# Kernel optimization log

Measured on AMD Instinct MI355X. Metric: run time of the kernel, lower is better.

Reference implementation:

```python
import jax, jax.numpy as jnp
import numpy as np

# Representation: lvals=[0,1] -> nreps NL=2, dim DIM=1+3=4; mult=8; kqv conv out_mult=3*mult
N, K, EDGE_DIM, HID = 10000, 16, 32, 64
MULT, NL, DIM = 8, 2, 4
OUT_MULT = 3 * MULT
E = N * K
NHEADS = 4
HEAD_DIM = MULT * DIM // NHEADS  # 8


def setup_inputs() -> dict:
    key = jax.random.key(0)
    ks = jax.random.split(key, 9)
    out_flat = NL * NL * MULT * OUT_MULT  # 768
    return {
        "basis1": jax.random.normal(ks[0], (E, DIM, NL), jnp.float32),
        "basis2": jax.random.normal(ks[1], (E, NL, DIM), jnp.float32),
        "edge_feats": jax.random.normal(ks[2], (E, EDGE_DIM), jnp.float32),
        "f": jax.random.normal(ks[3], (N, MULT, DIM), jnp.float32),
        "W1": jax.random.normal(ks[4], (HID, EDGE_DIM), jnp.float32) / np.sqrt(EDGE_DIM).astype(np.float32),
        "b1": jnp.zeros((HID,), jnp.float32),
        "W2": jax.random.normal(ks[5], (out_flat, HID), jnp.float32) / np.sqrt(HID).astype(np.float32),
        "b2": jnp.zeros((out_flat,), jnp.float32),
        "neighbor_idx": jax.random.randint(ks[6], (N, K), 0, N, dtype=jnp.int32),
    }


def reference(basis1, basis2, edge_feats, f, W1, b1, W2, b2, neighbor_idx):
    src = neighbor_idx.reshape(-1)  # (E,) source node per edge
    # RadialWeight: 2-layer MLP edge_feats -> per-edge TP weights (E, NL*OUT_MULT, NL*MULT)
    h = jax.nn.relu(edge_feats @ W1.T + b1)
    rw = (h @ W2.T + b2).reshape(E, NL * OUT_MULT, NL * MULT)
    # EquivariantConvolution: gather + small batched matmuls
    f_src = f[src]  # (E, MULT, DIM)
    tmp = jnp.einsum('emd,edl->eml', f_src, basis1).reshape(E, NL * MULT, 1)
    tmp = (rw @ tmp).reshape(E, OUT_MULT, NL)
    kqv = jnp.einsum('eml,eld->emd', tmp, basis2)  # (E, 3*MULT, DIM)
    # split fused k/q/v along multiplicity (repr_h.rep2.mult = 3*mult)
    k_, q_, v_ = jnp.split(kqv.reshape(N, K, OUT_MULT, DIM), 3, axis=2)  # each (N,K,MULT,DIM)
    k_ = k_.reshape(N, K, NHEADS, HEAD_DIM)
    v_ = v_.reshape(N, K, NHEADS, HEAD_DIM)
    q_node = q_.reshape(N, K, NHEADS, HEAD_DIM).mean(axis=1)  # per-node query (N,H,hd)
    scale = HEAD_DIM ** -0.5
    scores = jnp.einsum('nhd,nkhd->nhk', q_node, k_) * scale  # (N,H,K)
    w = jax.nn.softmax(scores, axis=-1)
    out = jnp.einsum('nhk,nkhd->nhd', w, v_)  # (N,H,hd)
    return out.reshape(N, MULT, DIM)
```

## Files before the change

kernel.cpp:

```cpp
#include <hip/hip_runtime.h>
#include <hip/hip_bf16.h>
#include <math.h>

#define N_NODES 10000
#define KNBR    16
#define EDGEF   32
#define HID     64
#define MULT    8
#define NL      2
#define DIM     4
#define OUT_MULT 24
#define NHEADS  4
#define HEAD_DIM 8
#define E_TOT   (N_NODES*KNBR)

#define EPB 128
#define TPB 256
#define NODES_PB 8
#define NSLICE 33

typedef float    f32x4 __attribute__((ext_vector_type(4)));
typedef _Float16 f16x8 __attribute__((ext_vector_type(8)));

#define BF1_HALVES (4*64*8)
#define BF2_HALVES (3*NSLICE*64*8)
#define WS_HALVES  (BF1_HALVES + BF2_HALVES)

__global__ __launch_bounds__(256)
void esa_prep(const float* __restrict__ W1, const float* __restrict__ W2,
              const float* __restrict__ b2, _Float16* __restrict__ wsh)
{
    int i = blockIdx.x * 256 + threadIdx.x;
    if (i >= WS_HALVES) return;
    float v;
    if (i < BF1_HALVES) {
        int j = i & 7, lane = (i >> 3) & 63, t = i >> 9;
        int k = ((lane >> 4) << 3) + j;
        int n = (t << 4) + (lane & 15);
        v = W1[n * EDGEF + k];
    } else {
        int i2 = i - BF1_HALVES;
        int j = i2 & 7, lane = (i2 >> 3) & 63;
        int st = i2 >> 9;
        int s = st % NSLICE, t = st / NSLICE;
        int k = (s << 5) + ((lane >> 4) << 3) + j;
        int n = (t << 4) + (lane & 15);
        if (k < 1024)      v = W2[(n * 16 + (k >> 6)) * HID + (k & 63)];
        else if (k < 1040) v = b2[n * 16 + (k - 1024)];
        else               v = 0.f;
    }
    wsh[i] = (_Float16)v;
}

__global__ __launch_bounds__(TPB)
void esa_main(const float* __restrict__ basis1, const float* __restrict__ basis2,
              const float* __restrict__ edge_feats, const float* __restrict__ f,
              const float* __restrict__ b1, const int* __restrict__ nbr,
              const _Float16* __restrict__ wsh, float* __restrict__ out)
{
    __shared__ __align__(16) unsigned char smem[53248];
    float*    t2  = (float*)smem;
    _Float16* hls = (_Float16*)(smem + 26624);
    _Float16* tpl = (_Float16*)(smem + 45056);
    float*    b2l = (float*)(smem + 49152);

    const int tid  = threadIdx.x;
    const int eb   = blockIdx.x * EPB;
    const int lane = tid & 63;
    const int w    = tid >> 6;
    const int lo   = lane & 15, hi = lane >> 4;

    {
        int el = tid >> 1, hf = tid & 1;
        int e  = eb + el;
        int src = nbr[e];
        const float4* b1p = (const float4*)(basis1 + (size_t)e * 8);
        float4 u0 = b1p[0], u1 = b1p[1];
        float bl0[4] = {u0.x, u0.z, u1.x, u1.z};
        float bl1[4] = {u0.y, u0.w, u1.y, u1.w};
        const float4* fp = (const float4*)(f + (size_t)src * 32 + hf * 16);
        _Float16 tpv[8];
        #pragma unroll
        for (int mm = 0; mm < 4; ++mm) {
            float4 fv = fp[mm];
            float a0 = fv.x*bl0[0] + fv.y*bl0[1] + fv.z*bl0[2] + fv.w*bl0[3];
            float a1 = fv.x*bl1[0] + fv.y*bl1[1] + fv.z*bl1[2] + fv.w*bl1[3];
            tpv[mm*2+0] = (_Float16)a0;
            tpv[mm*2+1] = (_Float16)a1;
        }
        *(f16x8*)(tpl + el*16 + hf*8) = *(f16x8*)tpv;
        float4 b2v = ((const float4*)(basis2 + (size_t)e * 8))[hf];
        *((float4*)(b2l + el*8) + hf) = b2v;
    }

    {
        float b1v[4];
        #pragma unroll
        for (int t = 0; t < 4; ++t) b1v[t] = b1[t*16 + lo];
        f16x8 afr[2];
        #pragma unroll
        for (int mt = 0; mt < 2; ++mt) {
            size_t eg = (size_t)(eb + w*32 + mt*16 + lo);
            const float4* p = (const float4*)(edge_feats + eg*32 + hi*8);
            float4 x0 = p[0], x1 = p[1];
            f16x8 a;
            a[0]=(_Float16)x0.x; a[1]=(_Float16)x0.y; a[2]=(_Float16)x0.z; a[3]=(_Float16)x0.w;
            a[4]=(_Float16)x1.x; a[5]=(_Float16)x1.y; a[6]=(_Float16)x1.z; a[7]=(_Float16)x1.w;
            afr[mt] = a;
        }
        #pragma unroll
        for (int t = 0; t < 4; ++t) {
            f16x8 bfr = *(const f16x8*)(wsh + ((size_t)(t*64 + lane)) * 8);
            #pragma unroll
            for (int mt = 0; mt < 2; ++mt) {
                f32x4 acc = {0.f, 0.f, 0.f, 0.f};
                acc = __builtin_amdgcn_mfma_f32_16x16x32_f16(afr[mt], bfr, acc, 0, 0, 0);
                #pragma unroll
                for (int r = 0; r < 4; ++r) {
                    float hv = acc[r] + b1v[t];
                    hv = hv > 0.f ? hv : 0.f;
                    int el = w*32 + mt*16 + hi*4 + r;
                    hls[el*72 + t*16 + lo] = (_Float16)hv;
                }
            }
        }
    }
    __syncthreads();

    {
        f32x4 acc[2][3];
        #pragma unroll
        for (int mt = 0; mt < 2; ++mt)
            #pragma unroll
            for (int t = 0; t < 3; ++t)
                acc[mt][t] = (f32x4){0.f, 0.f, 0.f, 0.f};

        const _Float16* Bf2 = wsh + BF1_HALVES;
        const int e0 = w*32 + lo;
        const int e1 = e0 + 16;
        const _Float16* hp0 = hls + e0*72 + hi*8;
        const _Float16* hp1 = hls + e1*72 + hi*8;
        f16x8 tp0a = *(const f16x8*)(tpl + e0*16);
        f16x8 tp0b = *(const f16x8*)(tpl + e0*16 + 8);
        f16x8 tp1a = *(const f16x8*)(tpl + e1*16);
        f16x8 tp1b = *(const f16x8*)(tpl + e1*16 + 8);

        #pragma unroll
        for (int sp = 0; sp < 16; ++sp) {
            _Float16 t0 = (sp < 8) ? tp0a[sp & 7] : tp0b[sp & 7];
            _Float16 t1 = (sp < 8) ? tp1a[sp & 7] : tp1b[sp & 7];
            f16x8 ts0 = {t0,t0,t0,t0,t0,t0,t0,t0};
            f16x8 ts1 = {t1,t1,t1,t1,t1,t1,t1,t1};
            #pragma unroll
            for (int sh = 0; sh < 2; ++sh) {
                const int s = sp*2 + sh;
                f16x8 bfr[3];
                #pragma unroll
                for (int t = 0; t < 3; ++t)
                    bfr[t] = *(const f16x8*)(Bf2 + ((size_t)((t*NSLICE + s)*64 + lane)) * 8);
                f16x8 h0 = *(const f16x8*)(hp0 + sh*32);
                f16x8 h1 = *(const f16x8*)(hp1 + sh*32);
                f16x8 a0 = h0 * ts0;
                f16x8 a1 = h1 * ts1;
                #pragma unroll
                for (int t = 0; t < 3; ++t) {
                    acc[0][t] = __builtin_amdgcn_mfma_f32_16x16x32_f16(a0, bfr[t], acc[0][t], 0, 0, 0);
                    acc[1][t] = __builtin_amdgcn_mfma_f32_16x16x32_f16(a1, bfr[t], acc[1][t], 0, 0, 0);
                }
            }
        }
        {
            f16x8 z = {(_Float16)0,(_Float16)0,(_Float16)0,(_Float16)0,
                       (_Float16)0,(_Float16)0,(_Float16)0,(_Float16)0};
            f16x8 a0 = (hi == 0) ? tp0a : (hi == 1) ? tp0b : z;
            f16x8 a1 = (hi == 0) ? tp1a : (hi == 1) ? tp1b : z;
            #pragma unroll
            for (int t = 0; t < 3; ++t) {
                f16x8 bfr = *(const f16x8*)(Bf2 + ((size_t)((t*NSLICE + 32)*64 + lane)) * 8);
                acc[0][t] = __builtin_amdgcn_mfma_f32_16x16x32_f16(a0, bfr, acc[0][t], 0, 0, 0);
                acc[1][t] = __builtin_amdgcn_mfma_f32_16x16x32_f16(a1, bfr, acc[1][t], 0, 0, 0);
            }
        }
        #pragma unroll
        for (int mt = 0; mt < 2; ++mt)
            #pragma unroll
            for (int t = 0; t < 3; ++t)
                #pragma unroll
                for (int r = 0; r < 4; ++r)
                    t2[(w*32 + mt*16 + hi*4 + r)*52 + t*16 + lo] = acc[mt][t][r];
    }
    __syncthreads();

    const int kk = lane >> 2, hh = lane & 3;
    #pragma unroll
    for (int it = 0; it < 2; ++it) {
        int nl = it*4 + w;
        int node = blockIdx.x * NODES_PB + nl;
        int el = nl*16 + kk;
        const float* trow = t2 + el*52;
        float4 tk = *(const float4*)(trow + hh*4);
        float4 tq = *(const float4*)(trow + 16 + hh*4);
        float4 tv = *(const float4*)(trow + 32 + hh*4);
        float4 bl0 = *(const float4*)(b2l + el*8);
        float4 bl1 = *(const float4*)(b2l + el*8 + 4);
        float k8[8], q8[8], v8[8];
        const float* B0 = (const float*)&bl0;
        const float* B1 = (const float*)&bl1;
        #pragma unroll
        for (int d = 0; d < 4; ++d) {
            k8[d]   = tk.x*B0[d] + tk.y*B1[d];
            k8[4+d] = tk.z*B0[d] + tk.w*B1[d];
            q8[d]   = tq.x*B0[d] + tq.y*B1[d];
            q8[4+d] = tq.z*B0[d] + tq.w*B1[d];
            v8[d]   = tv.x*B0[d] + tv.y*B1[d];
            v8[4+d] = tv.z*B0[d] + tv.w*B1[d];
        }
        float qn[8];
        #pragma unroll
        for (int i = 0; i < 8; ++i) qn[i] = q8[i];
        #pragma unroll
        for (int m = 4; m <= 32; m <<= 1)
            #pragma unroll
            for (int i = 0; i < 8; ++i) qn[i] += __shfl_xor(qn[i], m);
        float s = 0.f;
        #pragma unroll
        for (int i = 0; i < 8; ++i) s += qn[i]*k8[i];
        s *= 0.0220970869120796f;

        float mx = s;
        #pragma unroll
        for (int m = 4; m <= 32; m <<= 1) mx = fmaxf(mx, __shfl_xor(mx, m));
        float ex = __expf(s - mx);
        float den = ex;
        #pragma unroll
        for (int m = 4; m <= 32; m <<= 1) den += __shfl_xor(den, m);
        float wgt = ex / den;

        float o[8];
        #pragma unroll
        for (int i = 0; i < 8; ++i) o[i] = wgt * v8[i];
        #pragma unroll
        for (int m = 4; m <= 32; m <<= 1)
            #pragma unroll
            for (int i = 0; i < 8; ++i) o[i] += __shfl_xor(o[i], m);
        if (kk == 0) {
            float4* dst = (float4*)(out + (size_t)node*32 + hh*8);
            dst[0] = make_float4(o[0], o[1], o[2], o[3]);
            dst[1] = make_float4(o[4], o[5], o[6], o[7]);
        }
    }
}

extern "C" void kernel_launch(void* const* d_in, const int* in_sizes, int n_in,
                              void* d_out, int out_size, void* d_ws, size_t ws_size,
                              hipStream_t stream) {
    const float* basis1     = (const float*)d_in[0];
    const float* basis2     = (const float*)d_in[1];
    const float* edge_feats = (const float*)d_in[2];
    const float* f          = (const float*)d_in[3];
    const float* W1         = (const float*)d_in[4];
    const float* b1         = (const float*)d_in[5];
    const float* W2         = (const float*)d_in[6];
    const float* b2         = (const float*)d_in[7];
    const int*   nbr        = (const int*)d_in[8];
    float* out = (float*)d_out;
    _Float16* wsh = (_Float16*)d_ws;

    esa_prep<<<(WS_HALVES + 255)/256, 256, 0, stream>>>(W1, W2, b2, wsh);
    esa_main<<<E_TOT/EPB, TPB, 0, stream>>>(basis1, basis2, edge_feats, f,
                                            b1, nbr, wsh, out);
}
```

Before: 117.7 us.

## Split fused kernel into GEMM kernel and attention kernel via global scratch

Splits the fused kernel into two. The GEMM kernel writes per-edge intermediate t2 (E×48 floats) to global workspace, and a separate attention kernel reads it back along with basis2. This cuts shared memory from 52 KB to 22 KB and sets launch bounds for 4 blocks per CU, aiming for higher occupancy. In exchange it adds about 19 MB of global write and read traffic plus an extra kernel launch.

```diff
diff --git a/kernel.cpp b/kernel.cpp
--- a/kernel.cpp
+++ b/kernel.cpp
@@ -16,7 +16,6 @@
 
 #define EPB 128
 #define TPB 256
-#define NODES_PB 8
 #define NSLICE 33
 
 typedef float    f32x4 __attribute__((ext_vector_type(4)));
@@ -25,6 +24,7 @@
 #define BF1_HALVES (4*64*8)
 #define BF2_HALVES (3*NSLICE*64*8)
 #define WS_HALVES  (BF1_HALVES + BF2_HALVES)
+#define T2_OFF     131072
 
 __global__ __launch_bounds__(256)
 void esa_prep(const float* __restrict__ W1, const float* __restrict__ W2,
@@ -52,17 +52,15 @@
     wsh[i] = (_Float16)v;
 }
 
-__global__ __launch_bounds__(TPB)
-void esa_main(const float* __restrict__ basis1, const float* __restrict__ basis2,
-              const float* __restrict__ edge_feats, const float* __restrict__ f,
-              const float* __restrict__ b1, const int* __restrict__ nbr,
-              const _Float16* __restrict__ wsh, float* __restrict__ out)
+__global__ __launch_bounds__(TPB, 4)
+void esa_gemm(const float* __restrict__ basis1, const float* __restrict__ edge_feats,
+              const float* __restrict__ f, const float* __restrict__ b1,
+              const int* __restrict__ nbr, const _Float16* __restrict__ wsh,
+              float* __restrict__ t2g)
 {
-    __shared__ __align__(16) unsigned char smem[53248];
-    float*    t2  = (float*)smem;
-    _Float16* hls = (_Float16*)(smem + 26624);
-    _Float16* tpl = (_Float16*)(smem + 45056);
-    float*    b2l = (float*)(smem + 49152);
+    __shared__ __align__(16) unsigned char smem[22528];
+    _Float16* hls = (_Float16*)smem;
+    _Float16* tpl = (_Float16*)(smem + 18432);
 
     const int tid  = threadIdx.x;
     const int eb   = blockIdx.x * EPB;
@@ -89,8 +87,6 @@
             tpv[mm*2+1] = (_Float16)a1;
         }
         *(f16x8*)(tpl + el*16 + hf*8) = *(f16x8*)tpv;
-        float4 b2v = ((const float4*)(basis2 + (size_t)e * 8))[hf];
-        *((float4*)(b2l + el*8) + hf) = b2v;
     }
 
     {
@@ -187,67 +183,72 @@
             for (int t = 0; t < 3; ++t)
                 #pragma unroll
                 for (int r = 0; r < 4; ++r)
-                    t2[(w*32 + mt*16 + hi*4 + r)*52 + t*16 + lo] = acc[mt][t][r];
-    }
-    __syncthreads();
-
-    const int kk = lane >> 2, hh = lane & 3;
-    #pragma unroll
-    for (int it = 0; it < 2; ++it) {
-        int nl = it*4 + w;
-        int node = blockIdx.x * NODES_PB + nl;
-        int el = nl*16 + kk;
-        const float* trow = t2 + el*52;
-        float4 tk = *(const float4*)(trow + hh*4);
-        float4 tq = *(const float4*)(trow + 16 + hh*4);
-        float4 tv = *(const float4*)(trow + 32 + hh*4);
-        float4 bl0 = *(const float4*)(b2l + el*8);
-        float4 bl1 = *(const float4*)(b2l + el*8 + 4);
-        float k8[8], q8[8], v8[8];
-        const float* B0 = (const float*)&bl0;
-        const float* B1 = (const float*)&bl1;
-        #pragma unroll
-        for (int d = 0; d < 4; ++d) {
-            k8[d]   = tk.x*B0[d] + tk.y*B1[d];
-            k8[4+d] = tk.z*B0[d] + tk.w*B1[d];
-            q8[d]   = tq.x*B0[d] + tq.y*B1[d];
-            q8[4+d] = tq.z*B0[d] + tq.w*B1[d];
-            v8[d]   = tv.x*B0[d] + tv.y*B1[d];
-            v8[4+d] = tv.z*B0[d] + tv.w*B1[d];
-        }
-        float qn[8];
-        #pragma unroll
-        for (int i = 0; i < 8; ++i) qn[i] = q8[i];
-        #pragma unroll
-        for (int m = 4; m <= 32; m <<= 1)
-            #pragma unroll
-            for (int i = 0; i < 8; ++i) qn[i] += __shfl_xor(qn[i], m);
-        float s = 0.f;
-        #pragma unroll
-        for (int i = 0; i < 8; ++i) s += qn[i]*k8[i];
-        s *= 0.0220970869120796f;
-
-        float mx = s;
-        #pragma unroll
-        for (int m = 4; m <= 32; m <<= 1) mx = fmaxf(mx, __shfl_xor(mx, m));
-        float ex = __expf(s - mx);
-        float den = ex;
-        #pragma unroll
-        for (int m = 4; m <= 32; m <<= 1) den += __shfl_xor(den, m);
-        float wgt = ex / den;
-
-        float o[8];
-        #pragma unroll
-        for (int i = 0; i < 8; ++i) o[i] = wgt * v8[i];
-        #pragma unroll
-        for (int m = 4; m <= 32; m <<= 1)
-            #pragma unroll
-            for (int i = 0; i < 8; ++i) o[i] += __shfl_xor(o[i], m);
-        if (kk == 0) {
-            float4* dst = (float4*)(out + (size_t)node*32 + hh*8);
-            dst[0] = make_float4(o[0], o[1], o[2], o[3]);
-            dst[1] = make_float4(o[4], o[5], o[6], o[7]);
-        }
+                    t2g[(size_t)(eb + w*32 + mt*16 + hi*4 + r)*48 + t*16 + lo] = acc[mt][t][r];
+    }
+}
+
+__global__ __launch_bounds__(256)
+void esa_attn(const float* __restrict__ t2g, const float* __restrict__ basis2,
+              float* __restrict__ out)
+{
+    const int tid  = threadIdx.x;
+    const int w    = tid >> 6;
+    const int lane = tid & 63;
+    const int node = blockIdx.x * 4 + w;
+    const int kk   = lane >> 2, hh = lane & 3;
+    const int e    = node * KNBR + kk;
+
+    const float* trow = t2g + (size_t)e * 48;
+    float4 tk = *(const float4*)(trow + hh*4);
+    float4 tq = *(const float4*)(trow + 16 + hh*4);
+    float4 tv = *(const float4*)(trow + 32 + hh*4);
+    float4 bl0 = *(const float4*)(basis2 + (size_t)e * 8);
+    float4 bl1 = *(const float4*)(basis2 + (size_t)e * 8 + 4);
+
+    float k8[8], q8[8], v8[8];
+    const float* B0 = (const float*)&bl0;
+    const float* B1 = (const float*)&bl1;
+    #pragma unroll
+    for (int d = 0; d < 4; ++d) {
+        k8[d]   = tk.x*B0[d] + tk.y*B1[d];
+        k8[4+d] = tk.z*B0[d] + tk.w*B1[d];
+        q8[d]   = tq.x*B0[d] + tq.y*B1[d];
+        q8[4+d] = tq.z*B0[d] + tq.w*B1[d];
+        v8[d]   = tv.x*B0[d] + tv.y*B1[d];
+        v8[4+d] = tv.z*B0[d] + tv.w*B1[d];
+    }
+    float qn[8];
+    #pragma unroll
+    for (int i = 0; i < 8; ++i) qn[i] = q8[i];
+    #pragma unroll
+    for (int m = 4; m <= 32; m <<= 1)
+        #pragma unroll
+        for (int i = 0; i < 8; ++i) qn[i] += __shfl_xor(qn[i], m);
+    float s = 0.f;
+    #pragma unroll
+    for (int i = 0; i < 8; ++i) s += qn[i]*k8[i];
+    s *= 0.0220970869120796f;
+
+    float mx = s;
+    #pragma unroll
+    for (int m = 4; m <= 32; m <<= 1) mx = fmaxf(mx, __shfl_xor(mx, m));
+    float ex = __expf(s - mx);
+    float den = ex;
+    #pragma unroll
+    for (int m = 4; m <= 32; m <<= 1) den += __shfl_xor(den, m);
+    float wgt = ex / den;
+
+    float o[8];
+    #pragma unroll
+    for (int i = 0; i < 8; ++i) o[i] = wgt * v8[i];
+    #pragma unroll
+    for (int m = 4; m <= 32; m <<= 1)
+        #pragma unroll
+        for (int i = 0; i < 8; ++i) o[i] += __shfl_xor(o[i], m);
+    if (kk == 0) {
+        float4* dst = (float4*)(out + (size_t)node*32 + hh*8);
+        dst[0] = make_float4(o[0], o[1], o[2], o[3]);
+        dst[1] = make_float4(o[4], o[5], o[6], o[7]);
     }
 }
 
@@ -265,8 +266,9 @@
     const int*   nbr        = (const int*)d_in[8];
     float* out = (float*)d_out;
     _Float16* wsh = (_Float16*)d_ws;
+    float* t2g = (float*)((char*)d_ws + T2_OFF);
 
     esa_prep<<<(WS_HALVES + 255)/256, 256, 0, stream>>>(W1, W2, b2, wsh);
-    esa_main<<<E_TOT/EPB, TPB, 0, stream>>>(basis1, basis2, edge_feats, f,
-                                            b1, nbr, wsh, out);
-}
+    esa_gemm<<<E_TOT/EPB, TPB, 0, stream>>>(basis1, edge_feats, f, b1, nbr, wsh, t2g);
+    esa_attn<<<N_NODES/4, 256, 0, stream>>>(t2g, basis2, out);
+}
```

Result: slower. 126.3 us (+7.4%).

## Stage second-layer weight fragments through double-buffered LDS via async global-to-LDS loads

Applied to the files above, without the earlier changes.

Instead of every wave fetching the same second-layer weight fragments from global memory inside the MFMA loop, the four waves now cooperatively copy chunks of slices into two LDS buffers with global_load_lds. The next chunk is prefetched while the current one is consumed, with a block barrier per chunk. The aim is to remove redundant per-wave global/L1 traffic and hide load latency behind the MFMAs. It also loads the hidden activations into registers once, remaps the shared-memory layout (the output tile now overlaps the dead hidden buffer), pads the basis2 stride, and requests 3 blocks per CU in launch bounds. The cost is extra barriers and reliance on correct wait semantics for the async LDS loads.

```diff
diff --git a/kernel.cpp b/kernel.cpp
--- a/kernel.cpp
+++ b/kernel.cpp
@@ -6,18 +6,14 @@
 #define KNBR    16
 #define EDGEF   32
 #define HID     64
-#define MULT    8
-#define NL      2
-#define DIM     4
-#define OUT_MULT 24
-#define NHEADS  4
-#define HEAD_DIM 8
 #define E_TOT   (N_NODES*KNBR)
 
 #define EPB 128
 #define TPB 256
 #define NODES_PB 8
 #define NSLICE 33
+#define CHUNK 4
+#define NCHUNK 8
 
 typedef float    f32x4 __attribute__((ext_vector_type(4)));
 typedef _Float16 f16x8 __attribute__((ext_vector_type(8)));
@@ -52,23 +48,39 @@
     wsh[i] = (_Float16)v;
 }
 
-__global__ __launch_bounds__(TPB)
+__device__ __forceinline__ void issue16(const _Float16* g, unsigned char* l) {
+    __builtin_amdgcn_global_load_lds(
+        (const __attribute__((address_space(1))) void*)g,
+        (__attribute__((address_space(3))) void*)(void*)l, 16, 0, 0);
+}
+
+__global__ __launch_bounds__(TPB, 3)
 void esa_main(const float* __restrict__ basis1, const float* __restrict__ basis2,
               const float* __restrict__ edge_feats, const float* __restrict__ f,
               const float* __restrict__ b1, const int* __restrict__ nbr,
               const _Float16* __restrict__ wsh, float* __restrict__ out)
 {
     __shared__ __align__(16) unsigned char smem[53248];
+    _Float16* hls = (_Float16*)(smem + 24576);
+    _Float16* tpl = (_Float16*)(smem + 43008);
+    float*    b2l = (float*)(smem + 47104);
     float*    t2  = (float*)smem;
-    _Float16* hls = (_Float16*)(smem + 26624);
-    _Float16* tpl = (_Float16*)(smem + 45056);
-    float*    b2l = (float*)(smem + 49152);
 
     const int tid  = threadIdx.x;
     const int eb   = blockIdx.x * EPB;
     const int lane = tid & 63;
     const int w    = tid >> 6;
     const int lo   = lane & 15, hi = lane >> 4;
+
+    const _Float16* Bf2 = wsh + BF1_HALVES;
+
+    #pragma unroll
+    for (int j = 0; j < 3; ++j) {
+        issue16(Bf2 + ((size_t)((j*NSLICE + (0*CHUNK + w))*64) + lane)*8,
+                smem + 0*12288 + (w*3 + j)*1024);
+        issue16(Bf2 + ((size_t)((j*NSLICE + (1*CHUNK + w))*64) + lane)*8,
+                smem + 1*12288 + (w*3 + j)*1024);
+    }
 
     {
         int el = tid >> 1, hf = tid & 1;
@@ -90,7 +102,7 @@
         }
         *(f16x8*)(tpl + el*16 + hf*8) = *(f16x8*)tpv;
         float4 b2v = ((const float4*)(basis2 + (size_t)e * 8))[hf];
-        *((float4*)(b2l + el*8) + hf) = b2v;
+        *((float4*)(b2l + el*12) + hf) = b2v;
     }
 
     {
@@ -127,68 +139,76 @@
     }
     __syncthreads();
 
+    f32x4 acc[2][3];
+    #pragma unroll
+    for (int mt = 0; mt < 2; ++mt)
+        #pragma unroll
+        for (int t = 0; t < 3; ++t)
+            acc[mt][t] = (f32x4){0.f, 0.f, 0.f, 0.f};
+
+    const int e0 = w*32 + lo, e1 = e0 + 16;
+    f16x8 tp0a = *(const f16x8*)(tpl + e0*16);
+    f16x8 tp0b = *(const f16x8*)(tpl + e0*16 + 8);
+    f16x8 tp1a = *(const f16x8*)(tpl + e1*16);
+    f16x8 tp1b = *(const f16x8*)(tpl + e1*16 + 8);
+    f16x8 h0f[2], h1f[2];
+    h0f[0] = *(const f16x8*)(hls + e0*72 + hi*8);
+    h0f[1] = *(const f16x8*)(hls + e0*72 + 32 + hi*8);
+    h1f[0] = *(const f16x8*)(hls + e1*72 + hi*8);
+    h1f[1] = *(const f16x8*)(hls + e1*72 + 32 + hi*8);
+
+    #pragma unroll
+    for (int c = 0; c < NCHUNK; ++c) {
+        const _Float16* buf = (const _Float16*)(smem + (c & 1)*12288);
+        #pragma unroll
+        for (int sc = 0; sc < CHUNK; ++sc) {
+            const int s  = c*CHUNK + sc;
+            const int cc = s >> 1;
+            const int sh = s & 1;
+            f16x8 bfr[3];
+            #pragma unroll
+            for (int t = 0; t < 3; ++t)
+                bfr[t] = *(const f16x8*)(buf + ((sc*3 + t)*64 + lane)*8);
+            _Float16 s0 = (cc < 8) ? tp0a[cc & 7] : tp0b[cc & 7];
+            _Float16 s1 = (cc < 8) ? tp1a[cc & 7] : tp1b[cc & 7];
+            f16x8 a0 = h0f[sh] * (f16x8){s0,s0,s0,s0,s0,s0,s0,s0};
+            f16x8 a1 = h1f[sh] * (f16x8){s1,s1,s1,s1,s1,s1,s1,s1};
+            #pragma unroll
+            for (int t = 0; t < 3; ++t) {
+                acc[0][t] = __builtin_amdgcn_mfma_f32_16x16x32_f16(a0, bfr[t], acc[0][t], 0, 0, 0);
+                acc[1][t] = __builtin_amdgcn_mfma_f32_16x16x32_f16(a1, bfr[t], acc[1][t], 0, 0, 0);
+            }
+        }
+        __syncthreads();
+        if (c + 2 < NCHUNK) {
+            const int s = (c + 2)*CHUNK + w;
+            #pragma unroll
+            for (int j = 0; j < 3; ++j)
+                issue16(Bf2 + ((size_t)((j*NSLICE + s)*64) + lane)*8,
+                        smem + (c & 1)*12288 + (w*3 + j)*1024);
+        }
+    }
+
     {
-        f32x4 acc[2][3];
-        #pragma unroll
-        for (int mt = 0; mt < 2; ++mt)
-            #pragma unroll
-            for (int t = 0; t < 3; ++t)
-                acc[mt][t] = (f32x4){0.f, 0.f, 0.f, 0.f};
-
-        const _Float16* Bf2 = wsh + BF1_HALVES;
-        const int e0 = w*32 + lo;
-        const int e1 = e0 + 16;
-        const _Float16* hp0 = hls + e0*72 + hi*8;
-        const _Float16* hp1 = hls + e1*72 + hi*8;
-        f16x8 tp0a = *(const f16x8*)(tpl + e0*16);
-        f16x8 tp0b = *(const f16x8*)(tpl + e0*16 + 8);
-        f16x8 tp1a = *(const f16x8*)(tpl + e1*16);
-        f16x8 tp1b = *(const f16x8*)(tpl + e1*16 + 8);
-
-        #pragma unroll
-        for (int sp = 0; sp < 16; ++sp) {
-            _Float16 t0 = (sp < 8) ? tp0a[sp & 7] : tp0b[sp & 7];
-            _Float16 t1 = (sp < 8) ? tp1a[sp & 7] : tp1b[sp & 7];
-            f16x8 ts0 = {t0,t0,t0,t0,t0,t0,t0,t0};
-            f16x8 ts1 = {t1,t1,t1,t1,t1,t1,t1,t1};
-            #pragma unroll
-            for (int sh = 0; sh < 2; ++sh) {
-                const int s = sp*2 + sh;
-                f16x8 bfr[3];
-                #pragma unroll
-                for (int t = 0; t < 3; ++t)
-                    bfr[t] = *(const f16x8*)(Bf2 + ((size_t)((t*NSLICE + s)*64 + lane)) * 8);
-                f16x8 h0 = *(const f16x8*)(hp0 + sh*32);
-                f16x8 h1 = *(const f16x8*)(hp1 + sh*32);
-                f16x8 a0 = h0 * ts0;
-                f16x8 a1 = h1 * ts1;
-                #pragma unroll
-                for (int t = 0; t < 3; ++t) {
-                    acc[0][t] = __builtin_amdgcn_mfma_f32_16x16x32_f16(a0, bfr[t], acc[0][t], 0, 0, 0);
-                    acc[1][t] = __builtin_amdgcn_mfma_f32_16x16x32_f16(a1, bfr[t], acc[1][t], 0, 0, 0);
-                }
-            }
-        }
-        {
-            f16x8 z = {(_Float16)0,(_Float16)0,(_Float16)0,(_Float16)0,
-                       (_Float16)0,(_Float16)0,(_Float16)0,(_Float16)0};
-            f16x8 a0 = (hi == 0) ? tp0a : (hi == 1) ? tp0b : z;
-            f16x8 a1 = (hi == 0) ? tp1a : (hi == 1) ? tp1b : z;
-            #pragma unroll
-            for (int t = 0; t < 3; ++t) {
-                f16x8 bfr = *(const f16x8*)(Bf2 + ((size_t)((t*NSLICE + 32)*64 + lane)) * 8);
-                acc[0][t] = __builtin_amdgcn_mfma_f32_16x16x32_f16(a0, bfr, acc[0][t], 0, 0, 0);
-                acc[1][t] = __builtin_amdgcn_mfma_f32_16x16x32_f16(a1, bfr, acc[1][t], 0, 0, 0);
-            }
-        }
-        #pragma unroll
-        for (int mt = 0; mt < 2; ++mt)
-            #pragma unroll
-            for (int t = 0; t < 3; ++t)
-                #pragma unroll
-                for (int r = 0; r < 4; ++r)
-                    t2[(w*32 + mt*16 + hi*4 + r)*52 + t*16 + lo] = acc[mt][t][r];
-    }
+        f16x8 z = {(_Float16)0,(_Float16)0,(_Float16)0,(_Float16)0,
+                   (_Float16)0,(_Float16)0,(_Float16)0,(_Float16)0};
+        f16x8 a0 = (hi == 0) ? tp0a : (hi == 1) ? tp0b : z;
+        f16x8 a1 = (hi == 0) ? tp1a : (hi == 1) ? tp1b : z;
+        #pragma unroll
+        for (int t = 0; t < 3; ++t) {
+            f16x8 bfr = *(const f16x8*)(Bf2 + ((size_t)((t*NSLICE + 32)*64 + lane)) * 8);
+            acc[0][t] = __builtin_amdgcn_mfma_f32_16x16x32_f16(a0, bfr, acc[0][t], 0, 0, 0);
+            acc[1][t] = __builtin_amdgcn_mfma_f32_16x16x32_f16(a1, bfr, acc[1][t], 0, 0, 0);
+        }
+    }
+
+    #pragma unroll
+    for (int mt = 0; mt < 2; ++mt)
+        #pragma unroll
+        for (int t = 0; t < 3; ++t)
+            #pragma unroll
+            for (int r = 0; r < 4; ++r)
+                t2[(w*32 + mt*16 + hi*4 + r)*52 + t*16 + lo] = acc[mt][t][r];
     __syncthreads();
 
     const int kk = lane >> 2, hh = lane & 3;
@@ -201,8 +221,8 @@
         float4 tk = *(const float4*)(trow + hh*4);
         float4 tq = *(const float4*)(trow + 16 + hh*4);
         float4 tv = *(const float4*)(trow + 32 + hh*4);
-        float4 bl0 = *(const float4*)(b2l + el*8);
-        float4 bl1 = *(const float4*)(b2l + el*8 + 4);
+        float4 bl0 = *(const float4*)(b2l + el*12);
+        float4 bl1 = *(const float4*)(b2l + el*12 + 4);
         float k8[8], q8[8], v8[8];
         const float* B0 = (const float*)&bl0;
         const float* B1 = (const float*)&bl1;
```

Result: faster. 111.6 us (-5.1%).
